# Kernel tuning notes

Measured on AMD Instinct MI355X. Metric: run time of the kernel, lower is better.

## Reference

```python
import jax, jax.numpy as jnp
import numpy as np

B, S, D = 2, 2048, 1024
H, KVH, HD = 16, 4, 64


def setup_inputs() -> dict:
    key = jax.random.key(0)
    ks = jax.random.split(key, 7)
    return {
        "hidden_states": jax.random.normal(ks[0], (B, S, D), jnp.float32),
        "full_mask": jax.random.normal(ks[1], (B, 1, S, S), jnp.float32),
        "tag_mask": jax.random.normal(ks[2], (B, 1, S, S), jnp.float32),
        "wq": jax.random.normal(ks[3], (H * HD, D), jnp.float32) * 0.02,
        "wk": jax.random.normal(ks[4], (KVH * HD, D), jnp.float32) * 0.02,
        "wv": jax.random.normal(ks[5], (KVH * HD, D), jnp.float32) * 0.02,
        "wo": jax.random.normal(ks[6], (D, H * HD), jnp.float32) * 0.02,
    }


def _masked_sdpa(q, k, v, mask):
    # q,k,v: [B, h, S, HD]; mask: [B, 1, S, S] additive bias
    scale = 1.0 / jnp.sqrt(jnp.asarray(HD, q.dtype))
    w = jnp.einsum("bhqd,bhkd->bhqk", q, k) * scale + mask
    w = jax.nn.softmax(w.astype(jnp.float32), axis=-1).astype(q.dtype)
    return jnp.einsum("bhqk,bhkd->bhqd", w, v)


def _repeat_kv(x, n_rep):
    # [B, KVh, S, HD] -> [B, KVh*n_rep, S, HD]
    if n_rep == 1:
        return x
    return jnp.repeat(x, n_rep, axis=1)


def reference(hidden_states, full_mask, tag_mask, wq, wk, wv, wo):
    x = hidden_states
    q = (x @ wq.T).reshape(B, S, H, HD).transpose(0, 2, 1, 3)      # bhsd
    k = (x @ wk.T).reshape(B, S, KVH, HD).transpose(0, 2, 1, 3)
    v = (x @ wv.T).reshape(B, S, KVH, HD).transpose(0, 2, 1, 3)

    n_gq, n_lq = H // 2, H - H // 2
    n_gkv, n_lkv = KVH // 2, KVH - KVH // 2
    q_g, q_l = q[:, :n_gq], q[:, n_gq:]
    k_g, k_l = k[:, :n_gkv], k[:, n_gkv:]
    v_g, v_l = v[:, :n_gkv], v[:, n_gkv:]

    k_g = _repeat_kv(k_g, n_gq // n_gkv)
    v_g = _repeat_kv(v_g, n_gq // n_gkv)
    k_l = _repeat_kv(k_l, n_lq // n_lkv)
    v_l = _repeat_kv(v_l, n_lq // n_lkv)

    out_g = _masked_sdpa(q_g, k_g, v_g, full_mask)
    out_l = _masked_sdpa(q_l, k_l, v_l, tag_mask)
    attn = jnp.concatenate([out_g, out_l], axis=1)                  # [B,H,S,HD]
    attn = attn.transpose(0, 2, 1, 3).reshape(B, S, H * HD)
    return attn @ wo.T
```

## Files before the change

kernel.cpp:

```cpp
#include <hip/hip_runtime.h>
#include <hip/hip_bf16.h>

#define B_ 2
#define S_ 2048
#define D_ 1024
#define H_ 16
#define KVH_ 4
#define HD_ 64

#define LOG2E 1.44269504089f
#define QSCALE 0.18033688011f

typedef __attribute__((ext_vector_type(4))) float f32x4;
typedef __attribute__((ext_vector_type(16))) float f32x16;
typedef __attribute__((ext_vector_type(8))) short short8;

#define DEV static __device__ __forceinline__

DEV unsigned short f2bf(float f) {
  union { float f; unsigned int u; } v; v.f = f;
  unsigned int r = v.u + 0x7FFFu + ((v.u >> 16) & 1u);
  return (unsigned short)(r >> 16);
}

DEV float fexp2(float x) {
#if __has_builtin(__builtin_amdgcn_exp2f)
  return __builtin_amdgcn_exp2f(x);
#else
  float r;
  asm("v_exp_f32 %0, %1" : "=v"(r) : "v"(x));
  return r;
#endif
}

DEV unsigned int pack_bf16(float lo, float hi) {
  float2 f2; f2.x = lo; f2.y = hi;
  __hip_bfloat162 h2 = __float22bfloat162_rn(f2);
  union { __hip_bfloat162 h; unsigned int u; } cv;
  cv.h = h2;
  return cv.u;
}

DEV void gload_lds16(const void* g, void* l) {
  __builtin_amdgcn_global_load_lds(
      (const __attribute__((address_space(1))) unsigned int*)g,
      (__attribute__((address_space(3))) unsigned int*)l, 16, 0, 0);
}

__global__ __launch_bounds__(256) void cast_kernel(const float* __restrict__ src,
                                                   unsigned short* __restrict__ dst, int n4) {
  int i = blockIdx.x * 256 + threadIdx.x;
  if (i >= n4) return;
  float4 v = ((const float4*)src)[i];
  ushort4 o;
  o.x = f2bf(v.x); o.y = f2bf(v.y); o.z = f2bf(v.z); o.w = f2bf(v.w);
  ((ushort4*)dst)[i] = o;
}

template <int MODE>
__global__ __launch_bounds__(256) void gemm_bt(
    const unsigned short* __restrict__ A, const unsigned short* __restrict__ Bw,
    float* __restrict__ C, unsigned short* __restrict__ qb,
    unsigned short* __restrict__ kb, unsigned short* __restrict__ vb,
    int M, int N, int K, int ntn) {
  __shared__ __align__(16) unsigned short As[128 * 64];
  __shared__ __align__(16) unsigned short Bs[128 * 64];
  const int tid = threadIdx.x;
  const int lane = tid & 63, wid = tid >> 6;
  const int wr = wid >> 1, wc = wid & 1;
  const int tm = blockIdx.x / ntn, tn = blockIdx.x % ntn;
  const int row0 = tm * 128, col0 = tn * 128;
  f32x4 acc[4][4] = {};
  const int sr = tid >> 3, sc = (tid & 7) * 8;
  for (int kt = 0; kt < K; kt += 64) {
    __syncthreads();
#pragma unroll
    for (int i = 0; i < 4; ++i) {
      gload_lds16(A + (size_t)(row0 + i * 32 + sr) * K + kt + sc,
                  (void*)(As + i * 2048 + tid * 8));
      gload_lds16(Bw + (size_t)(col0 + i * 32 + sr) * K + kt + sc,
                  (void*)(Bs + i * 2048 + tid * 8));
    }
    __syncthreads();
#pragma unroll
    for (int ks = 0; ks < 64; ks += 32) {
      const int fc = ks + (lane >> 4) * 8;
      short8 af[4], bf[4];
#pragma unroll
      for (int m = 0; m < 4; ++m)
        af[m] = *(const short8*)&As[(wr * 64 + m * 16 + (lane & 15)) * 64 + fc];
#pragma unroll
      for (int n = 0; n < 4; ++n)
        bf[n] = *(const short8*)&Bs[(wc * 64 + n * 16 + (lane & 15)) * 64 + fc];
#pragma unroll
      for (int m = 0; m < 4; ++m)
#pragma unroll
        for (int n = 0; n < 4; ++n)
          acc[m][n] = __builtin_amdgcn_mfma_f32_16x16x32_bf16(af[m], bf[n], acc[m][n], 0, 0, 0);
    }
  }
#pragma unroll
  for (int m = 0; m < 4; ++m)
#pragma unroll
    for (int n = 0; n < 4; ++n)
#pragma unroll
      for (int j = 0; j < 4; ++j) {
        const int grow = row0 + wr * 64 + m * 16 + (lane >> 4) * 4 + j;
        const int gcol = col0 + wc * 64 + n * 16 + (lane & 15);
        const float v = acc[m][n][j];
        if (MODE == 0) {
          C[(size_t)grow * N + gcol] = v;
        } else {
          const int b = grow >> 11, s = grow & 2047;
          if (gcol < 1024) {
            const int hh = gcol >> 6, d = gcol & 63;
            qb[(((size_t)b * H_ + hh) * S_ + s) * HD_ + d] = f2bf(v * QSCALE);
          } else if (gcol < 1280) {
            const int kk = (gcol - 1024) >> 6, d = gcol & 63;
            kb[(((size_t)b * KVH_ + kk) * S_ + s) * HD_ + d] = f2bf(v);
          } else {
            const int kk = (gcol - 1280) >> 6, d = gcol & 63;
            vb[(((size_t)b * KVH_ + kk) * HD_ + d) * S_ + s] = f2bf(v);
          }
        }
      }
}

__global__ __launch_bounds__(256) void attn_kernel(
    const unsigned short* __restrict__ qb, const unsigned short* __restrict__ kb,
    const unsigned short* __restrict__ vb, const float* __restrict__ fmask,
    const float* __restrict__ tmask, unsigned short* __restrict__ attnb) {
  __shared__ __align__(16) unsigned short Ks[2][64 * 64];
  __shared__ __align__(16) unsigned short Vs[2][64 * 64];
  __shared__ __align__(16) float Ms[2][32 * 64];
  const int tid = threadIdx.x;
  const int lane = tid & 63, w = tid >> 6;
  const int l31 = lane & 31, hi = lane >> 5;

  const int swz = (blockIdx.x % 8) * 64 + blockIdx.x / 8;
  const int hh = swz & 1, qt = (swz >> 1) & 63, g = (swz >> 7) & 1, b = swz >> 8;
  const int h = g * 8 + hh * 4 + w;
  const int kvh = g * 2 + hh;

  const unsigned short* kbase = kb + ((size_t)b * KVH_ + kvh) * S_ * HD_;
  const unsigned short* vbase = vb + ((size_t)b * KVH_ + kvh) * S_ * HD_;
  const float* mbase = (g ? tmask : fmask) + (size_t)b * S_ * S_;

  short8 bq[4];
  {
    const unsigned short* qrow =
        qb + (((size_t)b * H_ + h) * S_ + qt * 32 + l31) * HD_;
#pragma unroll
    for (int ks = 0; ks < 4; ++ks)
      bq[ks] = *(const short8*)(qrow + ks * 16 + hi * 8);
  }

  f32x16 accO[2] = {};
  float mrow = -1e30f, lrow = 0.f;

  const int krow = tid >> 3, kblk = tid & 7;
  const int mrow_s = tid >> 4, mblk = tid & 15;

#define STAGE(KT, BUF)                                                                   \
  do {                                                                                   \
    gload_lds16(kbase + (size_t)((KT) + krow) * 64 + ((kblk ^ (krow & 7)) << 3),         \
                (void*)&Ks[BUF][tid * 8]);                                               \
    gload_lds16(kbase + (size_t)((KT) + 32 + krow) * 64 + ((kblk ^ (krow & 7)) << 3),    \
                (void*)&Ks[BUF][2048 + tid * 8]);                                        \
    gload_lds16(vbase + (size_t)krow * 2048 + (KT) + ((kblk ^ (krow & 7)) << 3),         \
                (void*)&Vs[BUF][tid * 8]);                                               \
    gload_lds16(vbase + (size_t)(32 + krow) * 2048 + (KT) + ((kblk ^ (krow & 7)) << 3),  \
                (void*)&Vs[BUF][2048 + tid * 8]);                                        \
    gload_lds16(mbase + (size_t)(qt * 32 + mrow_s) * 2048 + (KT) +                       \
                    ((mblk ^ (mrow_s & 15)) << 2),                                       \
                (void*)&Ms[BUF][tid * 4]);                                               \
    gload_lds16(mbase + (size_t)(qt * 32 + 16 + mrow_s) * 2048 + (KT) +                  \
                    ((mblk ^ (mrow_s & 15)) << 2),                                       \
                (void*)&Ms[BUF][1024 + tid * 4]);                                        \
  } while (0)

  STAGE(0, 0);
#pragma unroll 2
  for (int t = 0; t < 32; ++t) {
    const int cur = t & 1;
    if (t + 1 < 32) {
      STAGE((t + 1) * 64, cur ^ 1);
      asm volatile("s_waitcnt vmcnt(6)" ::: "memory");
    } else {
      asm volatile("s_waitcnt vmcnt(0)" ::: "memory");
    }
    __builtin_amdgcn_s_barrier();
    __builtin_amdgcn_sched_barrier(0);

    const unsigned short* ksb = Ks[cur];
    const unsigned short* vsb = Vs[cur];
    const float* msb = Ms[cur];

    f32x16 s[2] = {};
    __builtin_amdgcn_s_setprio(1);
#pragma unroll
    for (int u = 0; u < 2; ++u)
#pragma unroll
      for (int ks = 0; ks < 4; ++ks) {
        short8 ak = *(const short8*)&ksb[(u * 32 + l31) * 64 +
                                         (((ks * 2 + hi) ^ (lane & 7)) << 3)];
        s[u] = __builtin_amdgcn_mfma_f32_32x32x16_bf16(ak, bq[ks], s[u], 0, 0, 0);
      }
    __builtin_amdgcn_s_setprio(0);

    float tmax0 = -1e30f, tmax1 = -1e30f;
#pragma unroll
    for (int u = 0; u < 2; ++u)
#pragma unroll
      for (int rg = 0; rg < 4; ++rg) {
        f32x4 mk = *(const f32x4*)&msb[l31 * 64 +
                                       (((u * 8 + rg * 2 + hi) ^ (lane & 15)) << 2)];
        float v0 = fmaf(mk[0], LOG2E, s[u][rg * 4 + 0]);
        float v1 = fmaf(mk[1], LOG2E, s[u][rg * 4 + 1]);
        float v2 = fmaf(mk[2], LOG2E, s[u][rg * 4 + 2]);
        float v3 = fmaf(mk[3], LOG2E, s[u][rg * 4 + 3]);
        s[u][rg * 4 + 0] = v0;
        s[u][rg * 4 + 1] = v1;
        s[u][rg * 4 + 2] = v2;
        s[u][rg * 4 + 3] = v3;
        tmax0 = fmaxf(tmax0, fmaxf(v0, v1));
        tmax1 = fmaxf(tmax1, fmaxf(v2, v3));
      }
    float tmax = fmaxf(tmax0, tmax1);
    tmax = fmaxf(tmax, __shfl_xor(tmax, 32));

    if (__any(tmax > mrow + 11.5f)) {
      const float mnew = fmaxf(mrow, tmax);
      const float es = fexp2(mrow - mnew);
      mrow = mnew;
      lrow *= es;
#pragma unroll
      for (int r = 0; r < 16; ++r) {
        const float esb = __shfl(es, (r & 3) + 8 * (r >> 2) + 4 * hi);
        accO[0][r] *= esb;
        accO[1][r] *= esb;
      }
    }

    float rs0 = 0.f, rs1 = 0.f, rs2 = 0.f, rs3 = 0.f;
#pragma unroll
    for (int u = 0; u < 2; ++u)
#pragma unroll
      for (int r = 0; r < 16; r += 4) {
        float p0 = fexp2(s[u][r + 0] - mrow);
        float p1 = fexp2(s[u][r + 1] - mrow);
        float p2 = fexp2(s[u][r + 2] - mrow);
        float p3 = fexp2(s[u][r + 3] - mrow);
        s[u][r + 0] = p0; s[u][r + 1] = p1; s[u][r + 2] = p2; s[u][r + 3] = p3;
        rs0 += p0; rs1 += p1; rs2 += p2; rs3 += p3;
      }
    float rs = (rs0 + rs1) + (rs2 + rs3);
    rs += __shfl_xor(rs, 32);
    lrow += rs;

#pragma unroll
    for (int u = 0; u < 2; ++u) {
      unsigned int Dw[8], Sw[8];
#pragma unroll
      for (int i = 0; i < 8; ++i)
        Dw[i] = pack_bf16(s[u][2 * i], s[u][2 * i + 1]);
#pragma unroll
      for (int i = 0; i < 8; ++i)
        Sw[i] = (unsigned int)__shfl_xor((int)Dw[i], 32);
      short8 ap[2];
#pragma unroll
      for (int k2 = 0; k2 < 2; ++k2) {
        union { unsigned int wd[4]; short8 v; } cv;
        const int b0 = k2 * 4;
        cv.wd[0] = hi ? Sw[b0 + 2] : Dw[b0 + 0];
        cv.wd[1] = hi ? Sw[b0 + 3] : Dw[b0 + 1];
        cv.wd[2] = hi ? Dw[b0 + 2] : Sw[b0 + 0];
        cv.wd[3] = hi ? Dw[b0 + 3] : Sw[b0 + 1];
        ap[k2] = cv.v;
      }
      __builtin_amdgcn_s_setprio(1);
#pragma unroll
      for (int dt = 0; dt < 2; ++dt)
#pragma unroll
        for (int k2 = 0; k2 < 2; ++k2) {
          short8 bv = *(const short8*)&vsb[(dt * 32 + l31) * 64 +
                                           (((u * 4 + k2 * 2 + hi) ^ (lane & 7)) << 3)];
          accO[dt] = __builtin_amdgcn_mfma_f32_32x32x16_bf16(ap[k2], bv, accO[dt], 0, 0, 0);
        }
      __builtin_amdgcn_s_setprio(0);
    }
    __builtin_amdgcn_s_barrier();
    __builtin_amdgcn_sched_barrier(0);
  }
#undef STAGE

#pragma unroll
  for (int r = 0; r < 16; ++r) {
    const int crow = (r & 3) + 8 * (r >> 2) + 4 * hi;
    const float linv = 1.0f / __shfl(lrow, crow);
    const size_t o = (size_t)(b * S_ + qt * 32 + crow) * (H_ * HD_) + h * 64 + l31;
    attnb[o] = f2bf(accO[0][r] * linv);
    attnb[o + 32] = f2bf(accO[1][r] * linv);
  }
}

extern "C" void kernel_launch(void* const* d_in, const int* in_sizes, int n_in,
                              void* d_out, int out_size, void* d_ws, size_t ws_size,
                              hipStream_t stream) {
  (void)in_sizes; (void)n_in; (void)out_size; (void)ws_size;
  const float* x = (const float*)d_in[0];
  const float* fmask = (const float*)d_in[1];
  const float* tmask = (const float*)d_in[2];
  const float* wq = (const float*)d_in[3];
  const float* wk = (const float*)d_in[4];
  const float* wv = (const float*)d_in[5];
  const float* wo = (const float*)d_in[6];

  unsigned short* ws = (unsigned short*)d_ws;
  unsigned short* xb = ws;
  unsigned short* wqkvb = xb + (size_t)4096 * 1024;
  unsigned short* wob = wqkvb + (size_t)1536 * 1024;
  unsigned short* qbuf = wob + (size_t)1024 * 1024;
  unsigned short* kbuf = qbuf + (size_t)4096 * 1024;
  unsigned short* vbuf = kbuf + (size_t)1024 * 1024;
  unsigned short* attnb = vbuf + (size_t)1024 * 1024;

  cast_kernel<<<4096, 256, 0, stream>>>(x, xb, 1048576);
  cast_kernel<<<1024, 256, 0, stream>>>(wq, wqkvb, 262144);
  cast_kernel<<<256, 256, 0, stream>>>(wk, wqkvb + (size_t)1024 * 1024, 65536);
  cast_kernel<<<256, 256, 0, stream>>>(wv, wqkvb + (size_t)1280 * 1024, 65536);
  cast_kernel<<<1024, 256, 0, stream>>>(wo, wob, 262144);

  gemm_bt<1><<<32 * 12, 256, 0, stream>>>(xb, wqkvb, nullptr, qbuf, kbuf, vbuf,
                                          4096, 1536, 1024, 12);
  attn_kernel<<<512, 256, 0, stream>>>(qbuf, kbuf, vbuf, fmask, tmask, attnb);
  gemm_bt<0><<<32 * 8, 256, 0, stream>>>(attnb, wob, (float*)d_out,
                                         nullptr, nullptr, nullptr, 4096, 1024, 1024, 8);
}
```

Baseline: 151.5 us.

## Split key range across two wave groups per block and merge softmax partials

The attention block grows to 512 threads. Two groups of four waves each process half of the 2048-key range with their own double-buffered K/V LDS tiles. At the end the partial outputs and row max/sum are merged through LDS with a log-sum-exp rescale. The mask is now read from global memory straight into registers instead of being staged through LDS. This doubles the resident waves to hide latency and shortens the serial key loop, at the cost of a merge step, extra LDS use and higher register pressure under launch_bounds(512,4).

```diff
diff --git a/kernel.cpp b/kernel.cpp
--- a/kernel.cpp
+++ b/kernel.cpp
@@ -126,25 +126,28 @@
       }
 }
 
-__global__ __launch_bounds__(256) void attn_kernel(
+__global__ __launch_bounds__(512, 4) void attn_kernel(
     const unsigned short* __restrict__ qb, const unsigned short* __restrict__ kb,
     const unsigned short* __restrict__ vb, const float* __restrict__ fmask,
     const float* __restrict__ tmask, unsigned short* __restrict__ attnb) {
-  __shared__ __align__(16) unsigned short Ks[2][64 * 64];
-  __shared__ __align__(16) unsigned short Vs[2][64 * 64];
-  __shared__ __align__(16) float Ms[2][32 * 64];
+  __shared__ __align__(16) unsigned short Ks[2][2][64 * 64];
+  __shared__ __align__(16) unsigned short Vs[2][2][64 * 64];
   const int tid = threadIdx.x;
   const int lane = tid & 63, w = tid >> 6;
   const int l31 = lane & 31, hi = lane >> 5;
+  const int half = w >> 2, hd = w & 3;
 
   const int swz = (blockIdx.x % 8) * 64 + blockIdx.x / 8;
   const int hh = swz & 1, qt = (swz >> 1) & 63, g = (swz >> 7) & 1, b = swz >> 8;
-  const int h = g * 8 + hh * 4 + w;
+  const int h = g * 8 + hh * 4 + hd;
   const int kvh = g * 2 + hh;
 
-  const unsigned short* kbase = kb + ((size_t)b * KVH_ + kvh) * S_ * HD_;
-  const unsigned short* vbase = vb + ((size_t)b * KVH_ + kvh) * S_ * HD_;
-  const float* mbase = (g ? tmask : fmask) + (size_t)b * S_ * S_;
+  const unsigned short* kbase =
+      kb + ((size_t)b * KVH_ + kvh) * S_ * HD_ + (size_t)(half * 1024) * HD_;
+  const unsigned short* vbase =
+      vb + ((size_t)b * KVH_ + kvh) * HD_ * S_ + half * 1024;
+  const float* mline = (g ? tmask : fmask) +
+      ((size_t)b * S_ + qt * 32 + l31) * S_ + half * 1024;
 
   short8 bq[4];
   {
@@ -158,43 +161,46 @@
   f32x16 accO[2] = {};
   float mrow = -1e30f, lrow = 0.f;
 
-  const int krow = tid >> 3, kblk = tid & 7;
-  const int mrow_s = tid >> 4, mblk = tid & 15;
+  const int tl = tid & 255;
+  const int krow = tl >> 3, kblk = tl & 7;
 
 #define STAGE(KT, BUF)                                                                   \
   do {                                                                                   \
     gload_lds16(kbase + (size_t)((KT) + krow) * 64 + ((kblk ^ (krow & 7)) << 3),         \
-                (void*)&Ks[BUF][tid * 8]);                                               \
+                (void*)&Ks[half][BUF][tl * 8]);                                          \
     gload_lds16(kbase + (size_t)((KT) + 32 + krow) * 64 + ((kblk ^ (krow & 7)) << 3),    \
-                (void*)&Ks[BUF][2048 + tid * 8]);                                        \
+                (void*)&Ks[half][BUF][2048 + tl * 8]);                                   \
     gload_lds16(vbase + (size_t)krow * 2048 + (KT) + ((kblk ^ (krow & 7)) << 3),         \
-                (void*)&Vs[BUF][tid * 8]);                                               \
+                (void*)&Vs[half][BUF][tl * 8]);                                          \
     gload_lds16(vbase + (size_t)(32 + krow) * 2048 + (KT) + ((kblk ^ (krow & 7)) << 3),  \
-                (void*)&Vs[BUF][2048 + tid * 8]);                                        \
-    gload_lds16(mbase + (size_t)(qt * 32 + mrow_s) * 2048 + (KT) +                       \
-                    ((mblk ^ (mrow_s & 15)) << 2),                                       \
-                (void*)&Ms[BUF][tid * 4]);                                               \
-    gload_lds16(mbase + (size_t)(qt * 32 + 16 + mrow_s) * 2048 + (KT) +                  \
-                    ((mblk ^ (mrow_s & 15)) << 2),                                       \
-                (void*)&Ms[BUF][1024 + tid * 4]);                                        \
+                (void*)&Vs[half][BUF][2048 + tl * 8]);                                   \
   } while (0)
 
   STAGE(0, 0);
 #pragma unroll 2
-  for (int t = 0; t < 32; ++t) {
+  for (int t = 0; t < 16; ++t) {
     const int cur = t & 1;
-    if (t + 1 < 32) {
+    const int KT = t * 64;
+
+    f32x4 mk0[4], mk1[4];
+#pragma unroll
+    for (int rg = 0; rg < 4; ++rg)
+      mk0[rg] = *(const f32x4*)&mline[KT + rg * 8 + hi * 4];
+#pragma unroll
+    for (int rg = 0; rg < 4; ++rg)
+      mk1[rg] = *(const f32x4*)&mline[KT + 32 + rg * 8 + hi * 4];
+
+    if (t + 1 < 16) {
       STAGE((t + 1) * 64, cur ^ 1);
-      asm volatile("s_waitcnt vmcnt(6)" ::: "memory");
+      asm volatile("s_waitcnt vmcnt(12)" ::: "memory");
     } else {
-      asm volatile("s_waitcnt vmcnt(0)" ::: "memory");
+      asm volatile("s_waitcnt vmcnt(8)" ::: "memory");
     }
     __builtin_amdgcn_s_barrier();
     __builtin_amdgcn_sched_barrier(0);
 
-    const unsigned short* ksb = Ks[cur];
-    const unsigned short* vsb = Vs[cur];
-    const float* msb = Ms[cur];
+    const unsigned short* ksb = &Ks[half][cur][0];
+    const unsigned short* vsb = &Vs[half][cur][0];
 
     f32x16 s[2] = {};
     __builtin_amdgcn_s_setprio(1);
@@ -213,8 +219,7 @@
     for (int u = 0; u < 2; ++u)
 #pragma unroll
       for (int rg = 0; rg < 4; ++rg) {
-        f32x4 mk = *(const f32x4*)&msb[l31 * 64 +
-                                       (((u * 8 + rg * 2 + hi) ^ (lane & 15)) << 2)];
+        const f32x4 mk = u ? mk1[rg] : mk0[rg];
         float v0 = fmaf(mk[0], LOG2E, s[u][rg * 4 + 0]);
         float v1 = fmaf(mk[1], LOG2E, s[u][rg * 4 + 1]);
         float v2 = fmaf(mk[2], LOG2E, s[u][rg * 4 + 2]);
@@ -294,13 +299,39 @@
   }
 #undef STAGE
 
-#pragma unroll
-  for (int r = 0; r < 16; ++r) {
-    const int crow = (r & 3) + 8 * (r >> 2) + 4 * hi;
-    const float linv = 1.0f / __shfl(lrow, crow);
-    const size_t o = (size_t)(b * S_ + qt * 32 + crow) * (H_ * HD_) + h * 64 + l31;
-    attnb[o] = f2bf(accO[0][r] * linv);
-    attnb[o + 32] = f2bf(accO[1][r] * linv);
+  float* Of = (float*)&Ks[0][0][0];
+  float* mlf = (float*)&Vs[0][0][0];
+  __syncthreads();
+  if (half == 1) {
+#pragma unroll
+    for (int dt = 0; dt < 2; ++dt)
+#pragma unroll
+      for (int r = 0; r < 16; ++r) {
+        const int crow = (r & 3) + 8 * (r >> 2) + 4 * hi;
+        Of[hd * 2048 + crow * 64 + dt * 32 + l31] = accO[dt][r];
+      }
+    if (hi == 0) {
+      mlf[hd * 64 + l31 * 2 + 0] = mrow;
+      mlf[hd * 64 + l31 * 2 + 1] = lrow;
+    }
+  }
+  __syncthreads();
+  if (half == 0) {
+    const float m1 = mlf[hd * 64 + l31 * 2 + 0];
+    const float l1 = mlf[hd * 64 + l31 * 2 + 1];
+    const float M = fmaxf(mrow, m1);
+    const float w0 = fexp2(mrow - M), w1 = fexp2(m1 - M);
+    const float linv = 1.0f / (lrow * w0 + l1 * w1);
+    const float a0 = w0 * linv, a1 = w1 * linv;
+#pragma unroll
+    for (int r = 0; r < 16; ++r) {
+      const int crow = (r & 3) + 8 * (r >> 2) + 4 * hi;
+      const float a0c = __shfl(a0, crow);
+      const float a1c = __shfl(a1, crow);
+      const size_t o = (size_t)(b * S_ + qt * 32 + crow) * (H_ * HD_) + h * 64 + l31;
+      attnb[o] = f2bf(accO[0][r] * a0c + Of[hd * 2048 + crow * 64 + l31] * a1c);
+      attnb[o + 32] = f2bf(accO[1][r] * a0c + Of[hd * 2048 + crow * 64 + 32 + l31] * a1c);
+    }
   }
 }
 
@@ -333,7 +364,7 @@
 
   gemm_bt<1><<<32 * 12, 256, 0, stream>>>(xb, wqkvb, nullptr, qbuf, kbuf, vbuf,
                                           4096, 1536, 1024, 12);
-  attn_kernel<<<512, 256, 0, stream>>>(qbuf, kbuf, vbuf, fmask, tmask, attnb);
+  attn_kernel<<<512, 512, 0, stream>>>(qbuf, kbuf, vbuf, fmask, tmask, attnb);
   gemm_bt<0><<<32 * 8, 256, 0, stream>>>(attnb, wob, (float*)d_out,
                                          nullptr, nullptr, nullptr, 4096, 1024, 1024, 8);
 }
```

Result: slower. 219.5 us (+44.8%).

## Split attention KV range in two and merge partials in a separate kernel

Applied to the files above, without the earlier changes.

Splits each attention block's key/value range into two halves, doubling the grid so more blocks run concurrently. Each half writes unnormalized fp32 partial outputs plus running max and sum to workspace. A new merge kernel rescales and combines the two halves, normalizes, and writes the bf16 attention output. This trades extra global memory traffic and an additional launch for better occupancy and parallelism in the attention stage.

```diff
diff --git a/kernel.cpp b/kernel.cpp
--- a/kernel.cpp
+++ b/kernel.cpp
@@ -10,6 +10,9 @@
 
 #define LOG2E 1.44269504089f
 #define QSCALE 0.18033688011f
+
+#define PO_HALF ((size_t)B_ * H_ * S_ * HD_)
+#define PML_HALF ((size_t)B_ * H_ * S_ * 2)
 
 typedef __attribute__((ext_vector_type(4))) float f32x4;
 typedef __attribute__((ext_vector_type(16))) float f32x16;
@@ -129,7 +132,8 @@
 __global__ __launch_bounds__(256) void attn_kernel(
     const unsigned short* __restrict__ qb, const unsigned short* __restrict__ kb,
     const unsigned short* __restrict__ vb, const float* __restrict__ fmask,
-    const float* __restrict__ tmask, unsigned short* __restrict__ attnb) {
+    const float* __restrict__ tmask, float* __restrict__ pO,
+    float* __restrict__ pml) {
   __shared__ __align__(16) unsigned short Ks[2][64 * 64];
   __shared__ __align__(16) unsigned short Vs[2][64 * 64];
   __shared__ __align__(16) float Ms[2][32 * 64];
@@ -137,14 +141,17 @@
   const int lane = tid & 63, w = tid >> 6;
   const int l31 = lane & 31, hi = lane >> 5;
 
-  const int swz = (blockIdx.x % 8) * 64 + blockIdx.x / 8;
-  const int hh = swz & 1, qt = (swz >> 1) & 63, g = (swz >> 7) & 1, b = swz >> 8;
+  const int swz = (blockIdx.x % 8) * 128 + blockIdx.x / 8;
+  const int hh = swz & 1, qt = (swz >> 1) & 63, half = (swz >> 7) & 1;
+  const int g = (swz >> 8) & 1, b = swz >> 9;
   const int h = g * 8 + hh * 4 + w;
   const int kvh = g * 2 + hh;
 
-  const unsigned short* kbase = kb + ((size_t)b * KVH_ + kvh) * S_ * HD_;
-  const unsigned short* vbase = vb + ((size_t)b * KVH_ + kvh) * S_ * HD_;
-  const float* mbase = (g ? tmask : fmask) + (size_t)b * S_ * S_;
+  const unsigned short* kbase =
+      kb + (((size_t)b * KVH_ + kvh) * S_ + half * 1024) * HD_;
+  const unsigned short* vbase =
+      vb + ((size_t)b * KVH_ + kvh) * HD_ * S_ + half * 1024;
+  const float* mbase = (g ? tmask : fmask) + (size_t)b * S_ * S_ + half * 1024;
 
   short8 bq[4];
   {
@@ -181,9 +188,9 @@
 
   STAGE(0, 0);
 #pragma unroll 2
-  for (int t = 0; t < 32; ++t) {
+  for (int t = 0; t < 16; ++t) {
     const int cur = t & 1;
-    if (t + 1 < 32) {
+    if (t + 1 < 16) {
       STAGE((t + 1) * 64, cur ^ 1);
       asm volatile("s_waitcnt vmcnt(6)" ::: "memory");
     } else {
@@ -294,14 +301,45 @@
   }
 #undef STAGE
 
+  float* pOh = pO + half * PO_HALF + (((size_t)b * H_ + h) * S_ + qt * 32) * HD_;
 #pragma unroll
   for (int r = 0; r < 16; ++r) {
     const int crow = (r & 3) + 8 * (r >> 2) + 4 * hi;
-    const float linv = 1.0f / __shfl(lrow, crow);
-    const size_t o = (size_t)(b * S_ + qt * 32 + crow) * (H_ * HD_) + h * 64 + l31;
-    attnb[o] = f2bf(accO[0][r] * linv);
-    attnb[o + 32] = f2bf(accO[1][r] * linv);
-  }
+    pOh[crow * 64 + l31] = accO[0][r];
+    pOh[crow * 64 + 32 + l31] = accO[1][r];
+  }
+  if (hi == 0) {
+    float* pmlh = pml + half * PML_HALF + (((size_t)b * H_ + h) * S_ + qt * 32 + l31) * 2;
+    pmlh[0] = mrow;
+    pmlh[1] = lrow;
+  }
+}
+
+__global__ __launch_bounds__(256) void merge_kernel(
+    const float* __restrict__ pO, const float* __restrict__ pml,
+    unsigned short* __restrict__ attnb) {
+  const int idx = blockIdx.x * 256 + threadIdx.x;
+  const int d8 = (idx & 7) * 8;
+  const int row = idx >> 3;
+  const int s = row & 2047, hrow = (row >> 11) & 15, b = row >> 15;
+  const float m0 = pml[(size_t)row * 2 + 0], l0 = pml[(size_t)row * 2 + 1];
+  const float m1 = pml[PML_HALF + (size_t)row * 2 + 0];
+  const float l1 = pml[PML_HALF + (size_t)row * 2 + 1];
+  const float M = fmaxf(m0, m1);
+  const float w0 = fexp2(m0 - M), w1 = fexp2(m1 - M);
+  const float inv = 1.0f / (l0 * w0 + l1 * w1);
+  const float a0 = w0 * inv, a1 = w1 * inv;
+  const float* o0 = pO + (size_t)row * 64 + d8;
+  const float* o1 = pO + PO_HALF + (size_t)row * 64 + d8;
+  f32x4 x0 = *(const f32x4*)o0, x1 = *(const f32x4*)(o0 + 4);
+  f32x4 y0 = *(const f32x4*)o1, y1 = *(const f32x4*)(o1 + 4);
+  union { unsigned short us[8]; short8 v; } out;
+#pragma unroll
+  for (int j = 0; j < 4; ++j) {
+    out.us[j] = f2bf(x0[j] * a0 + y0[j] * a1);
+    out.us[4 + j] = f2bf(x1[j] * a0 + y1[j] * a1);
+  }
+  *(short8*)&attnb[(size_t)(b * S_ + s) * (H_ * HD_) + hrow * 64 + d8] = out.v;
 }
 
 extern "C" void kernel_launch(void* const* d_in, const int* in_sizes, int n_in,
@@ -324,6 +362,8 @@
   unsigned short* kbuf = qbuf + (size_t)4096 * 1024;
   unsigned short* vbuf = kbuf + (size_t)1024 * 1024;
   unsigned short* attnb = vbuf + (size_t)1024 * 1024;
+  float* pO = (float*)(attnb + (size_t)4096 * 1024);
+  float* pml = pO + 2 * PO_HALF;
 
   cast_kernel<<<4096, 256, 0, stream>>>(x, xb, 1048576);
   cast_kernel<<<1024, 256, 0, stream>>>(wq, wqkvb, 262144);
@@ -333,7 +373,8 @@
 
   gemm_bt<1><<<32 * 12, 256, 0, stream>>>(xb, wqkvb, nullptr, qbuf, kbuf, vbuf,
                                           4096, 1536, 1024, 12);
-  attn_kernel<<<512, 256, 0, stream>>>(qbuf, kbuf, vbuf, fmask, tmask, attnb);
+  attn_kernel<<<1024, 256, 0, stream>>>(qbuf, kbuf, vbuf, fmask, tmask, pO, pml);
+  merge_kernel<<<2048, 256, 0, stream>>>(pO, pml, attnb);
   gemm_bt<0><<<32 * 8, 256, 0, stream>>>(attnb, wob, (float*)d_out,
                                          nullptr, nullptr, nullptr, 4096, 1024, 1024, 8);
 }
```

Measured after the change: 160.3 us. 1.06x slower.
